# Kernel tuning notes

Hardware: AMD Instinct MI355X
Metric: run time of the kernel (lower is better)

## Reference

```python
import jax, jax.numpy as jnp
import numpy as np

EPS = 1e-6
HOPS = 3


def setup_inputs() -> dict:
    key = jax.random.key(0)
    ks = jax.random.split(key, 10)
    NA = NB = 50000
    E = 625000
    D = 128
    xA = jax.random.normal(ks[0], (NA, D), dtype=jnp.float32)
    xB = jax.random.normal(ks[1], (NB, D), dtype=jnp.float32)
    attAB = jax.random.uniform(ks[2], (E,), dtype=jnp.float32)
    attBA = jax.random.uniform(ks[3], (E,), dtype=jnp.float32)
    # AlphaCalculation params (xavier-ish small init per gain=0.02)
    fc1_w = jax.random.normal(ks[4], (D, D), dtype=jnp.float32) * 0.02
    fc1_b = jnp.zeros((D,), dtype=jnp.float32)
    fc2_w = jax.random.normal(ks[5], (1, D), dtype=jnp.float32) * 0.02
    fc2_b = jnp.zeros((1,), dtype=jnp.float32)
    eAB = jax.random.randint(ks[6], (2, E), 0, NA)  # src in A, dst in B
    eBA = jax.random.randint(ks[7], (2, E), 0, NB)  # src in B, dst in A
    return {"xA": xA, "xB": xB, "attAB": attAB, "attBA": attBA,
            "fc1_w": fc1_w, "fc1_b": fc1_b, "fc2_w": fc2_w, "fc2_b": fc2_b,
            "eAB": eAB, "eBA": eBA}


def _aggregate(edge_index, src_feat_all, attention, num_dst):
    # gather -> scale -> scatter-add
    msg = src_feat_all[edge_index[0]] * attention[:, None]  # [E, D]
    return jax.ops.segment_sum(msg, edge_index[1], num_segments=num_dst)


def reference(xA, xB, attAB, attBA, fc1_w, fc1_b, fc2_w, fc2_b, eAB, eBA):
    NA, NB = xA.shape[0], xB.shape[0]
    feat0A, feat0B = xA, xB
    # global embedding: mean over node types of per-type mean -> [1, D]
    g = 0.5 * (xA.mean(axis=0, keepdims=True) + xB.mean(axis=0, keepdims=True))
    # alpha = sigmoid(fc2(tanh(fc1(g)))).squeeze(-1), clamped
    h = jnp.tanh(g @ fc1_w.T + fc1_b)
    alpha = jax.nn.sigmoid(h @ fc2_w.T + fc2_b).squeeze(-1)  # [1]
    alpha = jnp.clip(alpha, EPS, 1.0 - EPS)
    curA, curB = feat0A, feat0B
    for _ in range(HOPS):
        # dst A receives from B via eBA; dst B receives from A via eAB
        msgA = _aggregate(eBA, curB, attBA, NA)
        msgB = _aggregate(eAB, curA, attAB, NB)
        newA = jnp.clip(feat0A * alpha + msgA * (1.0 - alpha), EPS, 1.0 / EPS)
        newB = jnp.clip(feat0B * alpha + msgB * (1.0 - alpha), EPS, 1.0 / EPS)
        curA, curB = newA, newB
    # concat node types for a single output array [NA+NB, D]
    return jnp.concatenate([curA, curB], axis=0)
```

## Files before the change

kernel.cpp:

```cpp
#include <hip/hip_runtime.h>
#include <math.h>

#define D 128
#define EPSV 1e-6f
#define CLIP_HI 1e6f
#define G 512
#define SLOTS 40
#define HCF 128
#define EPB 2048
#define RANGES 64
#define NCOMBO (2 * RANGES)
#define FBC2 8

typedef float v4f __attribute__((ext_vector_type(4)));
typedef float v2f __attribute__((ext_vector_type(2)));
typedef unsigned v4u __attribute__((ext_vector_type(4)));

__device__ __forceinline__ unsigned short f2bf(float f) {
    unsigned u = __float_as_uint(f);
    u = u + 0x7FFFu + ((u >> 16) & 1u);
    return (unsigned short)(u >> 16);
}
__device__ __forceinline__ void fma8v(uint4 u, float a, v2f* acc) {
    v2f a2 = {a, a};
    v2f p0 = {__uint_as_float(u.x << 16), __uint_as_float(u.x & 0xffff0000u)};
    v2f p1 = {__uint_as_float(u.y << 16), __uint_as_float(u.y & 0xffff0000u)};
    v2f p2 = {__uint_as_float(u.z << 16), __uint_as_float(u.z & 0xffff0000u)};
    v2f p3 = {__uint_as_float(u.w << 16), __uint_as_float(u.w & 0xffff0000u)};
    acc[0] += p0 * a2;
    acc[1] += p1 * a2;
    acc[2] += p2 * a2;
    acc[3] += p3 * a2;
}
__device__ __forceinline__ void unpack8(uint4 u, float* f) {
    f[0] = __uint_as_float(u.x << 16);
    f[1] = __uint_as_float(u.x & 0xffff0000u);
    f[2] = __uint_as_float(u.y << 16);
    f[3] = __uint_as_float(u.y & 0xffff0000u);
    f[4] = __uint_as_float(u.z << 16);
    f[5] = __uint_as_float(u.z & 0xffff0000u);
    f[6] = __uint_as_float(u.w << 16);
    f[7] = __uint_as_float(u.w & 0xffff0000u);
}
__device__ __forceinline__ float4 nt_load4f(const float* p) {
    v4f t = __builtin_nontemporal_load(reinterpret_cast<const v4f*>(p));
    return make_float4(t.x, t.y, t.z, t.w);
}
__device__ __forceinline__ void nt_store4f(float* p, float a, float b, float c, float d) {
    v4f t = {a, b, c, d};
    __builtin_nontemporal_store(t, reinterpret_cast<v4f*>(p));
}
__device__ __forceinline__ void nt_store4u(unsigned short* p, uint4 o) {
    v4u t = {o.x, o.y, o.z, o.w};
    __builtin_nontemporal_store(t, reinterpret_cast<v4u*>(p));
}
__device__ __forceinline__ long long nt_load_ll(const void* p) {
    return __builtin_nontemporal_load(reinterpret_cast<const long long*>(p));
}

__global__ __launch_bounds__(256) void colsum_bf16(
        const float* __restrict__ xA, const float* __restrict__ xB,
        int NA, int NB, float* __restrict__ partA, float* __restrict__ partB,
        unsigned short* __restrict__ tblA, unsigned short* __restrict__ tblB) {
    __shared__ float4 sh[256];
    int tid = threadIdx.x;
    int c4  = tid & 31;
    int rs  = tid >> 5;
    float4 sa = make_float4(0.f, 0.f, 0.f, 0.f);
    float4 sb = make_float4(0.f, 0.f, 0.f, 0.f);
    for (int r = blockIdx.x * 8 + rs; r < NA; r += gridDim.x * 8) {
        float4 v = nt_load4f(xA + (size_t)r * D + c4 * 4);
        sa.x += v.x; sa.y += v.y; sa.z += v.z; sa.w += v.w;
        ushort4 o; o.x = f2bf(v.x); o.y = f2bf(v.y); o.z = f2bf(v.z); o.w = f2bf(v.w);
        *reinterpret_cast<ushort4*>(tblA + (size_t)r * D + c4 * 4) = o;
    }
    for (int r = blockIdx.x * 8 + rs; r < NB; r += gridDim.x * 8) {
        float4 v = nt_load4f(xB + (size_t)r * D + c4 * 4);
        sb.x += v.x; sb.y += v.y; sb.z += v.z; sb.w += v.w;
        ushort4 o; o.x = f2bf(v.x); o.y = f2bf(v.y); o.z = f2bf(v.z); o.w = f2bf(v.w);
        *reinterpret_cast<ushort4*>(tblB + (size_t)r * D + c4 * 4) = o;
    }
    sh[tid] = sa; __syncthreads();
    if (tid < 128) { sh[tid].x += sh[tid+128].x; sh[tid].y += sh[tid+128].y; sh[tid].z += sh[tid+128].z; sh[tid].w += sh[tid+128].w; } __syncthreads();
    if (tid < 64)  { sh[tid].x += sh[tid+64].x;  sh[tid].y += sh[tid+64].y;  sh[tid].z += sh[tid+64].z;  sh[tid].w += sh[tid+64].w;  } __syncthreads();
    if (tid < 32)  {
        float4 t = sh[tid]; float4 u = sh[tid+32];
        t.x += u.x; t.y += u.y; t.z += u.z; t.w += u.w;
        *reinterpret_cast<float4*>(partA + (size_t)blockIdx.x * D + tid * 4) = t;
    }
    __syncthreads();
    sh[tid] = sb; __syncthreads();
    if (tid < 128) { sh[tid].x += sh[tid+128].x; sh[tid].y += sh[tid+128].y; sh[tid].z += sh[tid+128].z; sh[tid].w += sh[tid+128].w; } __syncthreads();
    if (tid < 64)  { sh[tid].x += sh[tid+64].x;  sh[tid].y += sh[tid+64].y;  sh[tid].z += sh[tid+64].z;  sh[tid].w += sh[tid+64].w;  } __syncthreads();
    if (tid < 32)  {
        float4 t = sh[tid]; float4 u = sh[tid+32];
        t.x += u.x; t.y += u.y; t.z += u.z; t.w += u.w;
        *reinterpret_cast<float4*>(partB + (size_t)blockIdx.x * D + tid * 4) = t;
    }
}

__global__ __launch_bounds__(1024) void compute_alpha(
        const float* __restrict__ partA, const float* __restrict__ partB,
        int NA, int NB,
        const float* __restrict__ fc1_w, const float* __restrict__ fc1_b,
        const float* __restrict__ fc2_w, const float* __restrict__ fc2_b,
        float* __restrict__ alpha_out) {
    __shared__ float redA[1024];
    __shared__ float redB[1024];
    __shared__ float g[D];
    __shared__ float h[D];
    int tid = threadIdx.x;
    int c = tid & 127;
    int slice = tid >> 7;
    float sa = 0.f, sb = 0.f;
    for (int b = slice; b < G; b += 8) {
        sa += partA[(size_t)b * D + c];
        sb += partB[(size_t)b * D + c];
    }
    redA[tid] = sa; redB[tid] = sb;
    __syncthreads();
    if (tid < 512) { redA[tid] += redA[tid + 512]; redB[tid] += redB[tid + 512]; } __syncthreads();
    if (tid < 256) { redA[tid] += redA[tid + 256]; redB[tid] += redB[tid + 256]; } __syncthreads();
    if (tid < 128) {
        float ta = redA[tid] + redA[tid + 128];
        float tb = redB[tid] + redB[tid + 128];
        g[c] = 0.5f * (ta / (float)NA + tb / (float)NB);
    }
    __syncthreads();
    if (tid < 128) {
        float acc = fc1_b[c];
        for (int k = 0; k < D; ++k) acc += g[k] * fc1_w[(size_t)c * D + k];
        h[c] = tanhf(acc);
    }
    __syncthreads();
    if (tid == 0) {
        float a = fc2_b[0];
        for (int k = 0; k < D; ++k) a += h[k] * fc2_w[k];
        a = 1.f / (1.f + expf(-a));
        a = fminf(fmaxf(a, EPSV), 1.f - EPSV);
        *alpha_out = a;
    }
}

__global__ __launch_bounds__(256) void partition_edges(
        const int* __restrict__ eA, const float* __restrict__ attA, int NA,
        const int* __restrict__ eB, const float* __restrict__ attB, int NB,
        int E, int2* __restrict__ queues, int* __restrict__ qcnt, int qcap) {
    __shared__ int lcnt[NCOMBO];
    __shared__ int lbase[NCOMBO];
    int tid = threadIdx.x;
    int nbl = gridDim.x >> 1;
    int dir = (int)(blockIdx.x >= (unsigned)nbl);
    int blk = dir ? (blockIdx.x - nbl) : blockIdx.x;
    const int* e = dir ? eB : eA;
    const float* att = dir ? attB : attA;
    unsigned divN = (unsigned)(((dir ? NB : NA) + RANGES - 1) / RANGES);
    if (divN == 0) divN = 1;
    int start = blk * EPB;

    if (tid < NCOMBO) lcnt[tid] = 0;
    __syncthreads();

    int dstv[8], srcv[8], lp[8];
    float attv[8];
    int cb[8];
    #pragma unroll
    for (int k = 0; k < 8; ++k) {
        int i = start + k * 256 + tid;
        if (i < E) {
            int dst = __builtin_nontemporal_load(&e[E + i]);
            dstv[k] = dst;
            srcv[k] = __builtin_nontemporal_load(&e[i]);
            attv[k] = __builtin_nontemporal_load(&att[i]);
            unsigned range = (unsigned)dst / divN;
            if (range > RANGES - 1) range = RANGES - 1;
            cb[k] = dir * RANGES + (int)range;
            lp[k] = atomicAdd(&lcnt[cb[k]], 1);
        } else {
            cb[k] = -1; lp[k] = 0; dstv[k] = 0; srcv[k] = 0; attv[k] = 0.f;
        }
    }
    __syncthreads();
    if (tid < NCOMBO) lbase[tid] = atomicAdd(&qcnt[tid], lcnt[tid]);
    __syncthreads();
    #pragma unroll
    for (int k = 0; k < 8; ++k) {
        if (cb[k] >= 0) {
            int pos = lbase[cb[k]] + lp[k];
            if (pos < qcap) {
                int2 v;
                v.x = (dstv[k] << 16) | (srcv[k] & 0xffff);
                v.y = __float_as_int(attv[k]);
                queues[(size_t)cb[k] * qcap + pos] = v;
            }
        }
    }
}

__global__ __launch_bounds__(256) void fill_from_queues(
        const int2* __restrict__ queues, const int* __restrict__ qcnt, int qcap,
        int* __restrict__ cntA, int2* __restrict__ ellA,
        int* __restrict__ cntB, int2* __restrict__ ellB) {
    int combo = blockIdx.x & (NCOMBO - 1);
    int chunk = blockIdx.x >> 7;
    int dir = combo >> 6;
    int* cnt  = dir ? cntB : cntA;
    int2* ell = dir ? ellB : ellA;
    int n = qcnt[combo];
    if (n > qcap) n = qcap;
    const int2* q = queues + (size_t)combo * qcap;
    for (int i = chunk * 256 + threadIdx.x; i < n; i += FBC2 * 256) {
        long long raw = nt_load_ll(&q[i]);
        int key = (int)(unsigned)raw;
        int dst = ((unsigned)key) >> 16;
        int src = key & 0xffff;
        int pos = atomicAdd(&cnt[dst], 1);
        if (pos < SLOTS) {
            int2 w; w.x = src; w.y = (int)(raw >> 32);
            ell[(size_t)dst * SLOTS + pos] = w;
        }
    }
}

__global__ __launch_bounds__(256) void fill_direct(
        const int* __restrict__ eA, const float* __restrict__ attA,
        int* __restrict__ cntA, int2* __restrict__ ellA, int NA,
        const int* __restrict__ eB, const float* __restrict__ attB,
        int* __restrict__ cntB, int2* __restrict__ ellB, int NB, int E) {
    int b = blockIdx.x;
    int combo = b & 15;
    int dir   = combo >> 3;
    int range = combo & 7;
    int chunk = b >> 4;
    const int* e; const float* att; int* cnt; int2* ell; int N;
    if (dir == 0) { e = eA; att = attA; cnt = cntA; ell = ellA; N = NA; }
    else          { e = eB; att = attB; cnt = cntB; ell = ellB; N = NB; }
    int lo = (int)((long)range * N >> 3), hi = (int)((long)(range + 1) * N >> 3);
    for (int i = chunk * 256 + threadIdx.x; i < E; i += HCF * 256) {
        int dst = __builtin_nontemporal_load(&e[E + i]);
        if (dst >= lo && dst < hi) {
            int pos = atomicAdd(&cnt[dst], 1);
            if (pos < SLOTS) {
                int2 v;
                v.x = __builtin_nontemporal_load(&e[i]);
                v.y = __float_as_int(__builtin_nontemporal_load(&att[i]));
                ell[(size_t)dst * SLOTS + pos] = v;
            }
        }
    }
}

template <int LAST>
__global__ __launch_bounds__(256) void aggregate6(
        const int* __restrict__ cntA, const int2* __restrict__ ellA,
        const unsigned short* __restrict__ gtA, const unsigned short* __restrict__ fxA,
        unsigned short* __restrict__ obfA, float* __restrict__ of32A, int NA,
        const int* __restrict__ cntB, const int2* __restrict__ ellB,
        const unsigned short* __restrict__ gtB, const unsigned short* __restrict__ fxB,
        unsigned short* __restrict__ obfB, float* __restrict__ of32B, int NB,
        const float* __restrict__ alpha_p) {
    int grp = blockIdx.x >> 3;
    int sub = blockIdx.x & 7;
    int rb  = grp * 4 + (sub & 3);
    int wid = threadIdx.x >> 6;
    int lane = threadIdx.x & 63;
    int g = lane >> 4;
    int l = lane & 15;
    const int* cnt; const int2* ellbase; const unsigned short* gt; const unsigned short* fx;
    unsigned short* obf; float* of32; int N;
    if (sub < 4) {
        cnt = cntA; ellbase = ellA; gt = gtA; fx = fxA;
        obf = obfA; of32 = of32A; N = NA;
    } else {
        cnt = cntB; ellbase = ellB; gt = gtB; fx = fxB;
        obf = obfB; of32 = of32B; N = NB;
    }
    int row = rb * 4 + wid;
    if (row >= N) return;
    int c = cnt[row];
    int deg = c < SLOTS ? c : SLOTS;
    const int2* ent = ellbase + (size_t)row * SLOTS;
    v2f acc2[4];
    acc2[0] = (v2f){0.f, 0.f}; acc2[1] = (v2f){0.f, 0.f};
    acc2[2] = (v2f){0.f, 0.f}; acc2[3] = (v2f){0.f, 0.f};
    int off = l * 8;

#define PROC16(BASE)                                                          \
    {                                                                         \
        unsigned sv[4]; float av[4]; uint4 u[4];                              \
        _Pragma("unroll")                                                     \
        for (int k = 0; k < 4; ++k) {                                         \
            int slot = (BASE) + k * 4 + g;                                    \
            long long rr = nt_load_ll(&ent[slot]);                            \
            bool valid = slot < deg;                                          \
            sv[k] = valid ? (unsigned)rr : 0u;                                \
            av[k] = valid ? __int_as_float((int)(rr >> 32)) : 0.0f;           \
        }                                                                     \
        _Pragma("unroll")                                                     \
        for (int k = 0; k < 4; ++k)                                           \
            u[k] = *reinterpret_cast<const uint4*>(gt + (size_t)sv[k] * D + off); \
        _Pragma("unroll")                                                     \
        for (int k = 0; k < 4; ++k) fma8v(u[k], av[k], acc2);                 \
    }

    PROC16(0);
    for (int base = 16; base < deg; base += 16) PROC16(base);
#undef PROC16

    float acc[8];
    #pragma unroll
    for (int k = 0; k < 4; ++k) { acc[2*k] = acc2[k][0]; acc[2*k+1] = acc2[k][1]; }
    #pragma unroll
    for (int k = 0; k < 8; ++k) {
        acc[k] += __shfl_xor(acc[k], 16);
        acc[k] += __shfl_xor(acc[k], 32);
    }
    if (g == 0) {
        float al = alpha_p[0], bl = 1.f - al;
        float fv[8];
        uint4 f = *reinterpret_cast<const uint4*>(fx + (size_t)row * D + off);
        unpack8(f, fv);
        float r[8];
        #pragma unroll
        for (int k = 0; k < 8; ++k)
            r[k] = fminf(fmaxf(fv[k] * al + acc[k] * bl, EPSV), CLIP_HI);
        if (LAST) {
            nt_store4f(of32 + (size_t)row * D + off,     r[0], r[1], r[2], r[3]);
            nt_store4f(of32 + (size_t)row * D + off + 4, r[4], r[5], r[6], r[7]);
        } else {
            uint4 o;
            o.x = (unsigned)f2bf(r[0]) | ((unsigned)f2bf(r[1]) << 16);
            o.y = (unsigned)f2bf(r[2]) | ((unsigned)f2bf(r[3]) << 16);
            o.z = (unsigned)f2bf(r[4]) | ((unsigned)f2bf(r[5]) << 16);
            o.w = (unsigned)f2bf(r[6]) | ((unsigned)f2bf(r[7]) << 16);
            nt_store4u(obf + (size_t)row * D + off, o);
        }
    }
}

__global__ void scatter_add(const float* __restrict__ cur, const float* __restrict__ att,
                            const int* __restrict__ edges, int E,
                            float* __restrict__ msg) {
    const long long total = (long long)E * (D / 4);
    long long stride = (long long)gridDim.x * blockDim.x;
    for (long long idx = (long long)blockIdx.x * blockDim.x + threadIdx.x;
         idx < total; idx += stride) {
        int e  = (int)(idx >> 5);
        int ch = (int)(idx & 31);
        int src = edges[e];
        int dst = edges[E + e];
        float a = att[e];
        const float4 v = *reinterpret_cast<const float4*>(cur + (size_t)src * D + ch * 4);
        float* p = msg + (size_t)dst * D + ch * 4;
        atomicAdd(p + 0, v.x * a);
        atomicAdd(p + 1, v.y * a);
        atomicAdd(p + 2, v.z * a);
        atomicAdd(p + 3, v.w * a);
    }
}

__global__ void combine(const float4* __restrict__ feat0, const float4* __restrict__ msg,
                        const float* __restrict__ alpha_p, float4* __restrict__ out, int n4) {
    float a = alpha_p[0];
    float b = 1.f - a;
    int stride = gridDim.x * blockDim.x;
    for (int i = blockIdx.x * blockDim.x + threadIdx.x; i < n4; i += stride) {
        float4 f = feat0[i];
        float4 m = msg[i];
        float4 r;
        r.x = fminf(fmaxf(f.x * a + m.x * b, EPSV), CLIP_HI);
        r.y = fminf(fmaxf(f.y * a + m.y * b, EPSV), CLIP_HI);
        r.z = fminf(fmaxf(f.z * a + m.z * b, EPSV), CLIP_HI);
        r.w = fminf(fmaxf(f.w * a + m.w * b, EPSV), CLIP_HI);
        out[i] = r;
    }
}

extern "C" void kernel_launch(void* const* d_in, const int* in_sizes, int n_in,
                              void* d_out, int out_size, void* d_ws, size_t ws_size,
                              hipStream_t stream) {
    const float* xA    = (const float*)d_in[0];
    const float* xB    = (const float*)d_in[1];
    const float* attAB = (const float*)d_in[2];
    const float* attBA = (const float*)d_in[3];
    const float* fc1_w = (const float*)d_in[4];
    const float* fc1_b = (const float*)d_in[5];
    const float* fc2_w = (const float*)d_in[6];
    const float* fc2_b = (const float*)d_in[7];
    const int*   eAB   = (const int*)d_in[8];
    const int*   eBA   = (const int*)d_in[9];

    const int NA = in_sizes[0] / D;
    const int NB = in_sizes[1] / D;
    const int E  = in_sizes[2];

    float* out  = (float*)d_out;
    float* outA = out;
    float* outB = out + (size_t)NA * D;

    const size_t TBL = (size_t)(NA + NB) * D;

    {
        unsigned short* tblP = (unsigned short*)d_ws;
        unsigned short* tblQ = tblP + TBL;
        unsigned short* xtab = tblQ + TBL;
        int2*  ellA  = (int2*)(xtab + TBL);
        int2*  ellB  = ellA + ((size_t)NA * SLOTS + 16);
        int*   cntA  = (int*)(ellB + ((size_t)NB * SLOTS + 16));
        int*   cntB  = cntA + NA;
        int*   qcnt  = cntB + NB;
        float* partA = (float*)(qcnt + NCOMBO);
        float* partB = partA + (size_t)G * D;
        float* alpha = partB + (size_t)G * D;
        size_t needed = (size_t)((char*)(alpha + 4) - (char*)d_ws);

        if (ws_size >= needed) {
            unsigned short* xtabA = xtab, *xtabB = xtab + (size_t)NA * D;
            unsigned short* tblPA = tblP, *tblPB = tblP + (size_t)NA * D;
            unsigned short* tblQA = tblQ, *tblQB = tblQ + (size_t)NA * D;

            colsum_bf16<<<G, 256, 0, stream>>>(xA, xB, NA, NB, partA, partB, xtabA, xtabB);
            compute_alpha<<<1, 1024, 0, stream>>>(partA, partB, NA, NB,
                                                  fc1_w, fc1_b, fc2_w, fc2_b, alpha);

            hipMemsetAsync(cntA, 0, ((size_t)NA + NB + NCOMBO) * sizeof(int), stream);

            int qcap = E / RANGES + E / (4 * RANGES) + 2048;
            bool small_idx = (NA < 65536) && (NB < 65536);
            bool qfit = (size_t)NCOMBO * (size_t)qcap * sizeof(int2)
                        <= (size_t)out_size * sizeof(float);
            if (small_idx && qfit) {
                int2* queues = (int2*)d_out;
                int nbl = (E + EPB - 1) / EPB;
                partition_edges<<<2 * nbl, 256, 0, stream>>>(
                    eBA, attBA, NA, eAB, attAB, NB, E, queues, qcnt, qcap);
                fill_from_queues<<<NCOMBO * FBC2, 256, 0, stream>>>(
                    queues, qcnt, qcap, cntA, ellA, cntB, ellB);
            } else {
                fill_direct<<<16 * HCF, 256, 0, stream>>>(
                    eBA, attBA, cntA, ellA, NA, eAB, attAB, cntB, ellB, NB, E);
            }

            int gA = (NA + 3) / 4, gB = (NB + 3) / 4;
            int gmax = gA > gB ? gA : gB;
            int grid = ((gmax + 3) / 4) * 8;
            aggregate6<0><<<grid, 256, 0, stream>>>(
                cntA, ellA, xtabB, xtabA, tblPA, nullptr, NA,
                cntB, ellB, xtabA, xtabB, tblPB, nullptr, NB, alpha);
            aggregate6<0><<<grid, 256, 0, stream>>>(
                cntA, ellA, tblPB, xtabA, tblQA, nullptr, NA,
                cntB, ellB, tblPA, xtabB, tblQB, nullptr, NB, alpha);
            aggregate6<1><<<grid, 256, 0, stream>>>(
                cntA, ellA, tblQB, xtabA, nullptr, outA, NA,
                cntB, ellB, tblQA, xtabB, nullptr, outB, NB, alpha);
            return;
        }
    }

    {
        float* msgA  = (float*)d_ws;
        float* msgB  = msgA + (size_t)NA * D;
        float* pA    = msgB + (size_t)NB * D;
        float* pB    = pA + (size_t)G * D;
        float* alph  = pB + (size_t)G * D;

        colsum_bf16<<<G, 256, 0, stream>>>(xA, xB, NA, NB, pA, pB,
                                           (unsigned short*)msgA, (unsigned short*)msgB);
        compute_alpha<<<1, 1024, 0, stream>>>(pA, pB, NA, NB,
                                              fc1_w, fc1_b, fc2_w, fc2_b, alph);

        const size_t msgBytes = ((size_t)NA + (size_t)NB) * D * sizeof(float);
        for (int hop = 0; hop < 3; ++hop) {
            hipMemsetAsync(msgA, 0, msgBytes, stream);
            const float* fA = (hop == 0) ? xA : outA;
            const float* fB = (hop == 0) ? xB : outB;
            scatter_add<<<4096, 256, 0, stream>>>(fB, attBA, eBA, E, msgA);
            scatter_add<<<4096, 256, 0, stream>>>(fA, attAB, eAB, E, msgB);
            combine<<<2048, 256, 0, stream>>>((const float4*)xA, (const float4*)msgA,
                                              alph, (float4*)outA, NA * D / 4);
            combine<<<2048, 256, 0, stream>>>((const float4*)xB, (const float4*)msgB,
                                              alph, (float4*)outB, NB * D / 4);
        }
    }
}
```

Before: 254.9 us.

## Split bf16 feature tables into 32-column chunks to keep gather working set cache-resident

Stores the bf16 feature tables in a column-chunked layout (four chunks of 32 columns each). Each hop then runs four aggregate7 launches, one per chunk, and every wave handles 16 neighbours at once with 4 lanes per row. The aim is to shrink the random-gather working set per launch (about 3.2 MB per table chunk) so it stays in L2/MALL and cuts DRAM traffic from scattered row reads. In exchange the edge list (ELL) and counts are re-read four times per hop, each gather fetches only 64 bytes, and there are more kernel launches.

```diff
diff --git a/kernel.cpp b/kernel.cpp
--- a/kernel.cpp
+++ b/kernel.cpp
@@ -11,6 +11,8 @@
 #define RANGES 64
 #define NCOMBO (2 * RANGES)
 #define FBC2 8
+#define NCHUNK 4
+#define CMAX 56000
 
 typedef float v4f __attribute__((ext_vector_type(4)));
 typedef float v2f __attribute__((ext_vector_type(2)));
@@ -61,24 +63,31 @@
 __global__ __launch_bounds__(256) void colsum_bf16(
         const float* __restrict__ xA, const float* __restrict__ xB,
         int NA, int NB, float* __restrict__ partA, float* __restrict__ partB,
-        unsigned short* __restrict__ tblA, unsigned short* __restrict__ tblB) {
+        unsigned short* __restrict__ tblA, unsigned short* __restrict__ tblB,
+        int chunked) {
     __shared__ float4 sh[256];
     int tid = threadIdx.x;
     int c4  = tid & 31;
     int rs  = tid >> 5;
+    int cb  = c4 >> 3;
+    int cc  = c4 & 7;
     float4 sa = make_float4(0.f, 0.f, 0.f, 0.f);
     float4 sb = make_float4(0.f, 0.f, 0.f, 0.f);
     for (int r = blockIdx.x * 8 + rs; r < NA; r += gridDim.x * 8) {
         float4 v = nt_load4f(xA + (size_t)r * D + c4 * 4);
         sa.x += v.x; sa.y += v.y; sa.z += v.z; sa.w += v.w;
         ushort4 o; o.x = f2bf(v.x); o.y = f2bf(v.y); o.z = f2bf(v.z); o.w = f2bf(v.w);
-        *reinterpret_cast<ushort4*>(tblA + (size_t)r * D + c4 * 4) = o;
+        size_t adr = chunked ? ((size_t)cb * NA * 32 + (size_t)r * 32 + cc * 4)
+                             : ((size_t)r * D + c4 * 4);
+        *reinterpret_cast<ushort4*>(tblA + adr) = o;
     }
     for (int r = blockIdx.x * 8 + rs; r < NB; r += gridDim.x * 8) {
         float4 v = nt_load4f(xB + (size_t)r * D + c4 * 4);
         sb.x += v.x; sb.y += v.y; sb.z += v.z; sb.w += v.w;
         ushort4 o; o.x = f2bf(v.x); o.y = f2bf(v.y); o.z = f2bf(v.z); o.w = f2bf(v.w);
-        *reinterpret_cast<ushort4*>(tblB + (size_t)r * D + c4 * 4) = o;
+        size_t adr = chunked ? ((size_t)cb * NB * 32 + (size_t)r * 32 + cc * 4)
+                             : ((size_t)r * D + c4 * 4);
+        *reinterpret_cast<ushort4*>(tblB + adr) = o;
     }
     sh[tid] = sa; __syncthreads();
     if (tid < 128) { sh[tid].x += sh[tid+128].x; sh[tid].y += sh[tid+128].y; sh[tid].z += sh[tid+128].z; sh[tid].w += sh[tid+128].w; } __syncthreads();
@@ -251,6 +260,90 @@
 }
 
 template <int LAST>
+__global__ __launch_bounds__(256) void aggregate7(
+        const int* __restrict__ cntA, const int2* __restrict__ ellA,
+        const unsigned short* __restrict__ gtA, const unsigned short* __restrict__ fxA,
+        unsigned short* __restrict__ obfA, float* __restrict__ of32A, int NA,
+        const int* __restrict__ cntB, const int2* __restrict__ ellB,
+        const unsigned short* __restrict__ gtB, const unsigned short* __restrict__ fxB,
+        unsigned short* __restrict__ obfB, float* __restrict__ of32B, int NB,
+        const float* __restrict__ alpha_p, int ck) {
+    int grp = blockIdx.x >> 3;
+    int sub = blockIdx.x & 7;
+    int rb  = grp * 4 + (sub & 3);
+    int wid = threadIdx.x >> 6;
+    int lane = threadIdx.x & 63;
+    int g = lane >> 2;
+    int l = lane & 3;
+    const int* cnt; const int2* ellbase; const unsigned short* gt; const unsigned short* fx;
+    unsigned short* obf; float* of32; int N;
+    if (sub < 4) {
+        cnt = cntA; ellbase = ellA; gt = gtA; fx = fxA;
+        obf = obfA; of32 = of32A; N = NA;
+    } else {
+        cnt = cntB; ellbase = ellB; gt = gtB; fx = fxB;
+        obf = obfB; of32 = of32B; N = NB;
+    }
+    int row = rb * 4 + wid;
+    if (row >= N) return;
+    int c = cnt[row];
+    int deg = c < SLOTS ? c : SLOTS;
+    const int2* ent = ellbase + (size_t)row * SLOTS;
+    v2f acc2[4];
+    acc2[0] = (v2f){0.f, 0.f}; acc2[1] = (v2f){0.f, 0.f};
+    acc2[2] = (v2f){0.f, 0.f}; acc2[3] = (v2f){0.f, 0.f};
+    int off = l * 8;
+
+#define PROC16C(BASE)                                                         \
+    {                                                                         \
+        int slot = (BASE) + g;                                                \
+        long long rr = nt_load_ll(&ent[slot]);                                \
+        bool valid = slot < deg;                                              \
+        unsigned sv = valid ? (unsigned)rr : 0u;                              \
+        float av = valid ? __int_as_float((int)(rr >> 32)) : 0.0f;            \
+        uint4 u = *reinterpret_cast<const uint4*>(gt + (size_t)sv * 32 + off);\
+        fma8v(u, av, acc2);                                                   \
+    }
+
+    PROC16C(0);
+    for (int base = 16; base < deg; base += 16) PROC16C(base);
+#undef PROC16C
+
+    float acc[8];
+    #pragma unroll
+    for (int k = 0; k < 4; ++k) { acc[2*k] = acc2[k][0]; acc[2*k+1] = acc2[k][1]; }
+    #pragma unroll
+    for (int k = 0; k < 8; ++k) {
+        acc[k] += __shfl_xor(acc[k], 4);
+        acc[k] += __shfl_xor(acc[k], 8);
+        acc[k] += __shfl_xor(acc[k], 16);
+        acc[k] += __shfl_xor(acc[k], 32);
+    }
+    if (g == 0) {
+        float al = alpha_p[0], bl = 1.f - al;
+        float fv[8];
+        uint4 f = *reinterpret_cast<const uint4*>(fx + (size_t)row * 32 + off);
+        unpack8(f, fv);
+        float r[8];
+        #pragma unroll
+        for (int k = 0; k < 8; ++k)
+            r[k] = fminf(fmaxf(fv[k] * al + acc[k] * bl, EPSV), CLIP_HI);
+        if (LAST) {
+            float* po = of32 + (size_t)row * D + ck * 32 + off;
+            nt_store4f(po,     r[0], r[1], r[2], r[3]);
+            nt_store4f(po + 4, r[4], r[5], r[6], r[7]);
+        } else {
+            uint4 o;
+            o.x = (unsigned)f2bf(r[0]) | ((unsigned)f2bf(r[1]) << 16);
+            o.y = (unsigned)f2bf(r[2]) | ((unsigned)f2bf(r[3]) << 16);
+            o.z = (unsigned)f2bf(r[4]) | ((unsigned)f2bf(r[5]) << 16);
+            o.w = (unsigned)f2bf(r[6]) | ((unsigned)f2bf(r[7]) << 16);
+            nt_store4u(obf + (size_t)row * 32 + off, o);
+        }
+    }
+}
+
+template <int LAST>
 __global__ __launch_bounds__(256) void aggregate6(
         const int* __restrict__ cntA, const int2* __restrict__ ellA,
         const unsigned short* __restrict__ gtA, const unsigned short* __restrict__ fxA,
@@ -419,40 +512,68 @@
             unsigned short* tblPA = tblP, *tblPB = tblP + (size_t)NA * D;
             unsigned short* tblQA = tblQ, *tblQB = tblQ + (size_t)NA * D;
 
-            colsum_bf16<<<G, 256, 0, stream>>>(xA, xB, NA, NB, partA, partB, xtabA, xtabB);
-            compute_alpha<<<1, 1024, 0, stream>>>(partA, partB, NA, NB,
-                                                  fc1_w, fc1_b, fc2_w, fc2_b, alpha);
-
-            hipMemsetAsync(cntA, 0, ((size_t)NA + NB + NCOMBO) * sizeof(int), stream);
-
             int qcap = E / RANGES + E / (4 * RANGES) + 2048;
             bool small_idx = (NA < 65536) && (NB < 65536);
             bool qfit = (size_t)NCOMBO * (size_t)qcap * sizeof(int2)
                         <= (size_t)out_size * sizeof(float);
-            if (small_idx && qfit) {
+            bool use_chunked = small_idx && qfit && (NA <= CMAX) && (NB <= CMAX);
+
+            colsum_bf16<<<G, 256, 0, stream>>>(xA, xB, NA, NB, partA, partB,
+                                               xtabA, xtabB, use_chunked ? 1 : 0);
+            compute_alpha<<<1, 1024, 0, stream>>>(partA, partB, NA, NB,
+                                                  fc1_w, fc1_b, fc2_w, fc2_b, alpha);
+
+            hipMemsetAsync(cntA, 0, ((size_t)NA + NB + NCOMBO) * sizeof(int), stream);
+
+            if (use_chunked) {
                 int2* queues = (int2*)d_out;
                 int nbl = (E + EPB - 1) / EPB;
                 partition_edges<<<2 * nbl, 256, 0, stream>>>(
                     eBA, attBA, NA, eAB, attAB, NB, E, queues, qcnt, qcap);
                 fill_from_queues<<<NCOMBO * FBC2, 256, 0, stream>>>(
                     queues, qcnt, qcap, cntA, ellA, cntB, ellB);
+
+                int gA = (NA + 3) / 4, gB = (NB + 3) / 4;
+                int gmax = gA > gB ? gA : gB;
+                int grid = ((gmax + 3) / 4) * 8;
+                size_t ca = (size_t)NA * 32, cbk = (size_t)NB * 32;
+                for (int ck = 0; ck < NCHUNK; ++ck) {
+                    aggregate7<0><<<grid, 256, 0, stream>>>(
+                        cntA, ellA, xtabB + ck * cbk, xtabA + ck * ca,
+                        tblPA + ck * ca, nullptr, NA,
+                        cntB, ellB, xtabA + ck * ca, xtabB + ck * cbk,
+                        tblPB + ck * cbk, nullptr, NB, alpha, ck);
+                }
+                for (int ck = 0; ck < NCHUNK; ++ck) {
+                    aggregate7<0><<<grid, 256, 0, stream>>>(
+                        cntA, ellA, tblPB + ck * cbk, xtabA + ck * ca,
+                        tblQA + ck * ca, nullptr, NA,
+                        cntB, ellB, tblPA + ck * ca, xtabB + ck * cbk,
+                        tblQB + ck * cbk, nullptr, NB, alpha, ck);
+                }
+                for (int ck = 0; ck < NCHUNK; ++ck) {
+                    aggregate7<1><<<grid, 256, 0, stream>>>(
+                        cntA, ellA, tblQB + ck * cbk, xtabA + ck * ca,
+                        nullptr, outA, NA,
+                        cntB, ellB, tblQA + ck * ca, xtabB + ck * cbk,
+                        nullptr, outB, NB, alpha, ck);
+                }
             } else {
                 fill_direct<<<16 * HCF, 256, 0, stream>>>(
                     eBA, attBA, cntA, ellA, NA, eAB, attAB, cntB, ellB, NB, E);
+                int gA = (NA + 3) / 4, gB = (NB + 3) / 4;
+                int gmax = gA > gB ? gA : gB;
+                int grid = ((gmax + 3) / 4) * 8;
+                aggregate6<0><<<grid, 256, 0, stream>>>(
+                    cntA, ellA, xtabB, xtabA, tblPA, nullptr, NA,
+                    cntB, ellB, xtabA, xtabB, tblPB, nullptr, NB, alpha);
+                aggregate6<0><<<grid, 256, 0, stream>>>(
+                    cntA, ellA, tblPB, xtabA, tblQA, nullptr, NA,
+                    cntB, ellB, tblPA, xtabB, tblQB, nullptr, NB, alpha);
+                aggregate6<1><<<grid, 256, 0, stream>>>(
+                    cntA, ellA, tblQB, xtabA, nullptr, outA, NA,
+                    cntB, ellB, tblQA, xtabB, nullptr, outB, NB, alpha);
             }
-
-            int gA = (NA + 3) / 4, gB = (NB + 3) / 4;
-            int gmax = gA > gB ? gA : gB;
-            int grid = ((gmax + 3) / 4) * 8;
-            aggregate6<0><<<grid, 256, 0, stream>>>(
-                cntA, ellA, xtabB, xtabA, tblPA, nullptr, NA,
-                cntB, ellB, xtabA, xtabB, tblPB, nullptr, NB, alpha);
-            aggregate6<0><<<grid, 256, 0, stream>>>(
-                cntA, ellA, tblPB, xtabA, tblQA, nullptr, NA,
-                cntB, ellB, tblPA, xtabB, tblQB, nullptr, NB, alpha);
-            aggregate6<1><<<grid, 256, 0, stream>>>(
-                cntA, ellA, tblQB, xtabA, nullptr, outA, NA,
-                cntB, ellB, tblQA, xtabB, nullptr, outB, NB, alpha);
             return;
         }
     }
@@ -465,7 +586,7 @@
         float* alph  = pB + (size_t)G * D;
 
         colsum_bf16<<<G, 256, 0, stream>>>(xA, xB, NA, NB, pA, pB,
-                                           (unsigned short*)msgA, (unsigned short*)msgB);
+                                           (unsigned short*)msgA, (unsigned short*)msgB, 0);
         compute_alpha<<<1, 1024, 0, stream>>>(pA, pB, NA, NB,
                                               fc1_w, fc1_b, fc2_w, fc2_b, alph);
 
```

New measurement: 557.2 us. 119% more time.
